# Optimization experiments

Measured on AMD Instinct MI355X. Metric: run time of the kernel, lower is better.

Reference implementation:

```python
import jax, jax.numpy as jnp
import numpy as np

B, C, H, W = 256, 200, 32, 32


def setup_inputs() -> dict:
    key = jax.random.key(0)
    x = jax.random.normal(key, (B, C, H, W), dtype=jnp.float32)
    # exact init of the torch nn.Parameter: log(3.2 / c^2) * ones(1,1)
    temperature = jnp.log(3.2 / (C * C)) * jnp.ones((1, 1), dtype=jnp.float32)
    return {"x": x, "temperature": temperature}


def reference(x, temperature):
    b, c, h, w = x.shape
    xf = x.reshape(b, c, h * w)                     # (B, c, hw)
    # Gram matrix x @ x^T  -> (B, c, c)
    G = jnp.einsum('bcm,bdm->bcd', xf, xf)
    # diagonal of G = squared norms per band  -> (B, c)
    d = jnp.einsum('bcm,bcm->bc', xf, xf)
    # I_M @ (G*I) puts d_j in every row; (G*I) @ I_M puts d_i in every column
    dcov = d[:, None, :] + d[:, :, None] - 2.0 * G  # (B, c, c)
    dcov = jnp.maximum(dcov, 0.0)
    dcov = jnp.sqrt(jnp.exp(temperature)[0, 0] * dcov + 1e-5)
    # double centering: dcov@I_M/c = row means, I_M@dcov/c = col means,
    # I_M@dcov@I_M/c^2 = global mean (per batch element)
    row_mean = jnp.mean(dcov, axis=2, keepdims=True)
    col_mean = jnp.mean(dcov, axis=1, keepdims=True)
    tot_mean = jnp.mean(dcov, axis=(1, 2), keepdims=True)
    return -(dcov - row_mean - col_mean + tot_mean)
```

## Files before the change

kernel.cpp:

```cpp
#include <hip/hip_runtime.h>
#include <hip/hip_bf16.h>

typedef __bf16 bf16x8 __attribute__((ext_vector_type(8)));
typedef float  f32x4  __attribute__((ext_vector_type(4)));

#define C_DIM   200
#define HW_DIM  1024
#define NT      13
#define PADC    208
#define BK      64
#define NKC     16
#define ROWB    128
#define TILEB   (PADC*ROWB)

__device__ __forceinline__ bf16x8 pack8(float4 a, float4 b){
  bf16x8 v;
  v[0]=(__bf16)a.x; v[1]=(__bf16)a.y; v[2]=(__bf16)a.z; v[3]=(__bf16)a.w;
  v[4]=(__bf16)b.x; v[5]=(__bf16)b.y; v[6]=(__bf16)b.z; v[7]=(__bf16)b.w;
  return v;
}

__global__ __launch_bounds__(832, 4)
void spectral_corr_kernel(const float* __restrict__ x,
                          const float* __restrict__ temp,
                          float* __restrict__ out)
{
  __shared__ __align__(16) char sA[2][TILEB];
  __shared__ float d_lds[PADC];
  __shared__ float rs_lds[PADC];

  const int tid = threadIdx.x;
  const int b   = blockIdx.x;
  const int w   = tid >> 6;
  const int l   = tid & 63;
  const int g   = l >> 4;
  const int c   = l & 15;

  const float* xb = x + (size_t)b * (C_DIM * HW_DIM);

  const int s0 = tid,        s1 = tid + 832;
  const int r0 = s0 >> 3,    ch0 = s0 & 7;
  const int r1 = s1 >> 3,    ch1 = s1 & 7;
  const int wo0 = r0*ROWB + ((ch0*16) ^ ((r0&7)<<4));
  const int wo1 = r1*ROWB + ((ch1*16) ^ ((r1&7)<<4));
  const bool v1 = (r1 < C_DIM);

  f32x4 acc[NT];
  #pragma unroll
  for (int j=0;j<NT;++j) acc[j] = (f32x4){0.f,0.f,0.f,0.f};

  {
    const float* p0 = xb + r0*HW_DIM + ch0*8;
    float4 a0 = *(const float4*)p0;
    float4 a1 = *(const float4*)(p0+4);
    float4 b0 = make_float4(0.f,0.f,0.f,0.f), b1 = b0;
    if (v1){
      const float* p1 = xb + r1*HW_DIM + ch1*8;
      b0 = *(const float4*)p1; b1 = *(const float4*)(p1+4);
    }
    *reinterpret_cast<bf16x8*>(&sA[0][wo0]) = pack8(a0,a1);
    *reinterpret_cast<bf16x8*>(&sA[0][wo1]) = pack8(b0,b1);
  }
  __syncthreads();

  const float et = expf(temp[0]);

  const int wrow = w*16 + c;
  const int wro  = wrow*ROWB;
  const int wsw  = (wrow&7)<<4;

  for (int kc = 0; kc < NKC; ++kc){
    const char* base = sA[kc & 1];
    float4 a0,a1,b0,b1;
    const bool pre = (kc+1 < NKC);
    if (pre){
      const float* p0 = xb + r0*HW_DIM + (kc+1)*BK + ch0*8;
      a0 = *(const float4*)p0; a1 = *(const float4*)(p0+4);
      if (v1){
        const float* p1 = xb + r1*HW_DIM + (kc+1)*BK + ch1*8;
        b0 = *(const float4*)p1; b1 = *(const float4*)(p1+4);
      } else { b0 = make_float4(0.f,0.f,0.f,0.f); b1 = b0; }
    }
    #pragma unroll
    for (int s = 0; s < 2; ++s){
      const int kb = s*64 + g*16;
      bf16x8 fw = *reinterpret_cast<const bf16x8*>(base + wro + (kb ^ wsw));
      #pragma unroll
      for (int j = 0; j < NT; ++j){
        const int row = j*16 + c;
        bf16x8 fj = *reinterpret_cast<const bf16x8*>(
                        base + row*ROWB + (kb ^ ((row&7)<<4)));
        acc[j] = __builtin_amdgcn_mfma_f32_16x16x32_bf16(fw, fj, acc[j], 0, 0, 0);
      }
    }
    if (pre){
      char* dst = sA[(kc+1)&1];
      *reinterpret_cast<bf16x8*>(&dst[wo0]) = pack8(a0,a1);
      *reinterpret_cast<bf16x8*>(&dst[wo1]) = pack8(b0,b1);
    }
    __syncthreads();
  }

  #pragma unroll
  for (int j=0;j<NT;++j){
    if (j == w){
      #pragma unroll
      for (int i=0;i<4;++i)
        if (c == g*4 + i) d_lds[j*16 + c] = acc[j][i];
    }
  }
  __syncthreads();

  float dr[4];
  #pragma unroll
  for (int i=0;i<4;++i) dr[i] = d_lds[w*16 + g*4 + i];
  float rsum[4] = {0.f,0.f,0.f,0.f};
  #pragma unroll
  for (int j=0;j<NT;++j){
    const float dc = d_lds[j*16 + c];
    const bool cv  = (j*16 + c) < C_DIM;
    #pragma unroll
    for (int i=0;i<4;++i){
      float v = dr[i] + dc - 2.0f*acc[j][i];
      v = fmaxf(v, 0.0f);
      v = sqrtf(fmaf(et, v, 1e-5f));
      acc[j][i] = v;
      if (cv) rsum[i] += v;
    }
  }
  #pragma unroll
  for (int m=1;m<16;m<<=1){
    #pragma unroll
    for (int i=0;i<4;++i) rsum[i] += __shfl_xor(rsum[i], m, 64);
  }
  if (c == 0){
    #pragma unroll
    for (int i=0;i<4;++i) rs_lds[w*16 + g*4 + i] = rsum[i];
  }
  __syncthreads();

  float tot = 0.f;
  for (int r=0;r<C_DIM;++r) tot += rs_lds[r];
  const float inv  = 1.0f/(float)C_DIM;
  const float totm = tot*inv*inv;

  float* ob = out + b*(C_DIM*C_DIM);
  float rmr[4];
  #pragma unroll
  for (int i=0;i<4;++i) rmr[i] = rs_lds[w*16 + g*4 + i]*inv;
  #pragma unroll
  for (int j=0;j<NT;++j){
    const int col = j*16 + c;
    if (col < C_DIM){
      const float rmc = rs_lds[col]*inv;
      #pragma unroll
      for (int i=0;i<4;++i){
        const int row = w*16 + g*4 + i;
        if (row < C_DIM)
          ob[row*C_DIM + col] = rmr[i] + rmc - totm - acc[j][i];
      }
    }
  }
}

extern "C" void kernel_launch(void* const* d_in, const int* in_sizes, int n_in,
                              void* d_out, int out_size, void* d_ws, size_t ws_size,
                              hipStream_t stream) {
  const float* x    = (const float*)d_in[0];
  const float* temp = (const float*)d_in[1];
  float* out        = (float*)d_out;
  spectral_corr_kernel<<<dim3(256), dim3(832), 0, stream>>>(x, temp, out);
}
```

Baseline: 311.3 us.

## Pre-convert slab to bf16 workspace and stream tiles via global_load_lds

Each block first converts its whole fp32 input slab to bf16 in a global workspace, then streams k-tiles into LDS with direct global-to-LDS 16-byte loads. This drops the register staging and per-tile conversion from the main loop and uses a simpler swizzled addressing. In exchange it adds a full extra write and read of the slab through global memory or L2. Rows 200..207 of the padded workspace are never written, so they may hold garbage that feeds padded MFMA rows, and there is no fence between the global writes and the later direct-to-LDS reads.

```diff
diff --git a/kernel.cpp b/kernel.cpp
--- a/kernel.cpp
+++ b/kernel.cpp
@@ -12,18 +12,17 @@
 #define NKC     16
 #define ROWB    128
 #define TILEB   (PADC*ROWB)
+#define SLAB    (PADC*HW_DIM)
 
-__device__ __forceinline__ bf16x8 pack8(float4 a, float4 b){
-  bf16x8 v;
-  v[0]=(__bf16)a.x; v[1]=(__bf16)a.y; v[2]=(__bf16)a.z; v[3]=(__bf16)a.w;
-  v[4]=(__bf16)b.x; v[5]=(__bf16)b.y; v[6]=(__bf16)b.z; v[7]=(__bf16)b.w;
-  return v;
-}
+#define GLD16(gp, lp) __builtin_amdgcn_global_load_lds(                      \
+    (const __attribute__((address_space(1))) unsigned int*)(gp),             \
+    (__attribute__((address_space(3))) unsigned int*)(lp), 16, 0, 0)
 
 __global__ __launch_bounds__(832, 4)
 void spectral_corr_kernel(const float* __restrict__ x,
                           const float* __restrict__ temp,
-                          float* __restrict__ out)
+                          float* __restrict__ out,
+                          __hip_bfloat16* __restrict__ ws)
 {
   __shared__ __align__(16) char sA[2][TILEB];
   __shared__ float d_lds[PADC];
@@ -36,67 +35,55 @@
   const int g   = l >> 4;
   const int c   = l & 15;
 
-  const float* xb = x + (size_t)b * (C_DIM * HW_DIM);
+  const float*    xb = x  + (size_t)b * (C_DIM * HW_DIM);
+  __hip_bfloat16* wb = ws + (size_t)b * SLAB;
 
-  const int s0 = tid,        s1 = tid + 832;
-  const int r0 = s0 >> 3,    ch0 = s0 & 7;
-  const int r1 = s1 >> 3,    ch1 = s1 & 7;
-  const int wo0 = r0*ROWB + ((ch0*16) ^ ((r0&7)<<4));
-  const int wo1 = r1*ROWB + ((ch1*16) ^ ((r1&7)<<4));
-  const bool v1 = (r1 < C_DIM);
+  for (int base = tid*8; base < C_DIM*HW_DIM; base += 832*8){
+    float4 a0 = *(const float4*)(xb + base);
+    float4 a1 = *(const float4*)(xb + base + 4);
+    bf16x8 v;
+    v[0]=(__bf16)a0.x; v[1]=(__bf16)a0.y; v[2]=(__bf16)a0.z; v[3]=(__bf16)a0.w;
+    v[4]=(__bf16)a1.x; v[5]=(__bf16)a1.y; v[6]=(__bf16)a1.z; v[7]=(__bf16)a1.w;
+    *reinterpret_cast<bf16x8*>(wb + base) = v;
+  }
+  __syncthreads();
+
+  const float et = expf(temp[0]);
+
+  const int si = l >> 3;
+  const int sc = (l & 7) ^ si;
+  const int i0 = 2*w, i1 = 2*w + 1;
+  const __hip_bfloat16* gs0 = wb + (size_t)(8*i0 + si)*HW_DIM + sc*8;
+  const __hip_bfloat16* gs1 = wb + (size_t)(8*i1 + si)*HW_DIM + sc*8;
 
   f32x4 acc[NT];
   #pragma unroll
   for (int j=0;j<NT;++j) acc[j] = (f32x4){0.f,0.f,0.f,0.f};
 
-  {
-    const float* p0 = xb + r0*HW_DIM + ch0*8;
-    float4 a0 = *(const float4*)p0;
-    float4 a1 = *(const float4*)(p0+4);
-    float4 b0 = make_float4(0.f,0.f,0.f,0.f), b1 = b0;
-    if (v1){
-      const float* p1 = xb + r1*HW_DIM + ch1*8;
-      b0 = *(const float4*)p1; b1 = *(const float4*)(p1+4);
-    }
-    *reinterpret_cast<bf16x8*>(&sA[0][wo0]) = pack8(a0,a1);
-    *reinterpret_cast<bf16x8*>(&sA[0][wo1]) = pack8(b0,b1);
-  }
+  GLD16(gs0, &sA[0][i0*1024]);
+  GLD16(gs1, &sA[0][i1*1024]);
   __syncthreads();
 
-  const float et = expf(temp[0]);
-
-  const int wrow = w*16 + c;
-  const int wro  = wrow*ROWB;
-  const int wsw  = (wrow&7)<<4;
+  const int swz = (c & 7) << 4;
+  const int rb0 = c*ROWB + ((     g*16) ^ swz);
+  const int rb1 = c*ROWB + ((64 + g*16) ^ swz);
 
   for (int kc = 0; kc < NKC; ++kc){
-    const char* base = sA[kc & 1];
-    float4 a0,a1,b0,b1;
-    const bool pre = (kc+1 < NKC);
-    if (pre){
-      const float* p0 = xb + r0*HW_DIM + (kc+1)*BK + ch0*8;
-      a0 = *(const float4*)p0; a1 = *(const float4*)(p0+4);
-      if (v1){
-        const float* p1 = xb + r1*HW_DIM + (kc+1)*BK + ch1*8;
-        b0 = *(const float4*)p1; b1 = *(const float4*)(p1+4);
-      } else { b0 = make_float4(0.f,0.f,0.f,0.f); b1 = b0; }
+    const char* bufc = sA[kc & 1];
+    if (kc+1 < NKC){
+      char* bufn = sA[(kc+1)&1];
+      GLD16(gs0 + (kc+1)*BK, &bufn[i0*1024]);
+      GLD16(gs1 + (kc+1)*BK, &bufn[i1*1024]);
     }
     #pragma unroll
     for (int s = 0; s < 2; ++s){
-      const int kb = s*64 + g*16;
-      bf16x8 fw = *reinterpret_cast<const bf16x8*>(base + wro + (kb ^ wsw));
+      const char* p = bufc + (s ? rb1 : rb0);
+      bf16x8 fw = *reinterpret_cast<const bf16x8*>(p + w*2048);
       #pragma unroll
       for (int j = 0; j < NT; ++j){
-        const int row = j*16 + c;
-        bf16x8 fj = *reinterpret_cast<const bf16x8*>(
-                        base + row*ROWB + (kb ^ ((row&7)<<4)));
+        bf16x8 fj = *reinterpret_cast<const bf16x8*>(p + j*2048);
         acc[j] = __builtin_amdgcn_mfma_f32_16x16x32_bf16(fw, fj, acc[j], 0, 0, 0);
       }
-    }
-    if (pre){
-      char* dst = sA[(kc+1)&1];
-      *reinterpret_cast<bf16x8*>(&dst[wo0]) = pack8(a0,a1);
-      *reinterpret_cast<bf16x8*>(&dst[wo1]) = pack8(b0,b1);
     }
     __syncthreads();
   }
@@ -169,5 +156,6 @@
   const float* x    = (const float*)d_in[0];
   const float* temp = (const float*)d_in[1];
   float* out        = (float*)d_out;
-  spectral_corr_kernel<<<dim3(256), dim3(832), 0, stream>>>(x, temp, out);
+  __hip_bfloat16* ws = (__hip_bfloat16*)d_ws;
+  spectral_corr_kernel<<<dim3(256), dim3(832), 0, stream>>>(x, temp, out, ws);
 }
```

New measurement: 354.0 us. 1.14x slower.
